# Kernel optimization log

Hardware: AMD Instinct MI355X
Metric: run time of the kernel (lower is better)

The kernel has to match this reference:

```python
import jax, jax.numpy as jnp
import numpy as np

N_NODES = 100000


def _gcn_norm(edge_index, edge_weight, n):
    # PyG gcn_norm: add self-loops (weight 1), symmetric normalization
    row, col = edge_index[0], edge_index[1]
    loop = jnp.arange(n, dtype=edge_index.dtype)
    row = jnp.concatenate([row, loop])
    col = jnp.concatenate([col, loop])
    ew = jnp.concatenate([edge_weight, jnp.ones((n,), edge_weight.dtype)])
    deg = jax.ops.segment_sum(ew, col, num_segments=n)
    dinv = jnp.where(deg > 0, jax.lax.rsqrt(deg), jnp.zeros_like(deg))
    norm = dinv[row] * ew * dinv[col]  # [E+N]
    return row, col, norm


def _gcn_layer(x, row, col, norm, W, b, n):
    h = x @ W                                   # [N, out] dense GEMM
    msg = norm[:, None] * h[row]                # gather + scale [E+N, out]
    out = jax.ops.segment_sum(msg, col, num_segments=n)  # scatter-add
    return out + b


def setup_inputs() -> dict:
    key = jax.random.key(0)
    ks = jax.random.split(key, 12)
    in_c, hid_c, out_c = 64, 128, 64
    E = 1600000
    x = jax.random.normal(ks[0], (N_NODES, in_c), jnp.float32)
    edge_index = jax.random.randint(ks[1], (2, E), 0, N_NODES, dtype=jnp.int64)
    edge_weight = jax.random.uniform(ks[2], (E,), jnp.float32)
    edge_label_index = jax.random.randint(ks[3], (2, 400000), 0, N_NODES, dtype=jnp.int64)

    def glorot(k, shape):
        lim = np.sqrt(6.0 / (shape[0] + shape[1])).astype(np.float32)
        return jax.random.uniform(k, shape, jnp.float32, -lim, lim)

    W_in = glorot(ks[4], (in_c, hid_c))
    b_in = jnp.zeros((hid_c,), jnp.float32)
    W_hid = jnp.stack([glorot(ks[5 + i], (hid_c, hid_c)) for i in range(4)])
    b_hid = jnp.zeros((4, hid_c), jnp.float32)
    W_out = glorot(ks[9], (hid_c, out_c))
    b_out = jnp.zeros((out_c,), jnp.float32)
    return {"x": x, "edge_index": edge_index, "edge_weight": edge_weight,
            "edge_label_index": edge_label_index,
            "W_in": W_in, "b_in": b_in, "W_hid": W_hid, "b_hid": b_hid,
            "W_out": W_out, "b_out": b_out}


def reference(x, edge_index, edge_weight, edge_label_index,
              W_in, b_in, W_hid, b_hid, W_out, b_out):
    n = x.shape[0]
    row, col, norm = _gcn_norm(edge_index, edge_weight, n)  # shared by all layers
    h = jax.nn.relu(_gcn_layer(x, row, col, norm, W_in, b_in, n))
    for i in range(W_hid.shape[0]):  # 4 hidden GCN layers
        h = jax.nn.relu(_gcn_layer(h, row, col, norm, W_hid[i], b_hid[i], n))
    enc = _gcn_layer(h, row, col, norm, W_out, b_out, n)  # [N, out_c]
    # dot-product link decoder
    logits = jnp.sum(enc[edge_label_index[0]] * enc[edge_label_index[1]], axis=1)
    return jax.nn.sigmoid(logits)
```

## Files before the change

### kernel.cpp

```cpp
#include <hip/hip_runtime.h>
#include <hip/hip_bf16.h>
#include <math.h>


using bf16x8 = __attribute__((ext_vector_type(8))) short;
using f32x4  = __attribute__((ext_vector_type(4))) float;

__device__ inline unsigned f2bf_bits(float f) {
    unsigned u = __float_as_uint(f);
    return (u + 0x7fffu + ((u >> 16) & 1u)) >> 16;
}
__device__ inline float bflo(unsigned w) { return __uint_as_float(w << 16); }
__device__ inline float bfhi(unsigned w) { return __uint_as_float(w & 0xffff0000u); }


__global__ void k_zero(int* __restrict__ hist, int n) {
    int i = blockIdx.x * 256 + threadIdx.x;
    if (i < n) hist[i] = 0;
}

__global__ void k_hist(const int* __restrict__ col, int* __restrict__ hist,
                       int* __restrict__ pos, int E) {
    int i = blockIdx.x * 256 + threadIdx.x;
    if (i < E) pos[i] = atomicAdd(&hist[col[i]], 1);
}

__global__ __launch_bounds__(256) void k_scan1(const int* __restrict__ hist,
                                               int* __restrict__ rowptr,
                                               int* __restrict__ bsum, int n) {
    __shared__ int lds[256];
    int t = threadIdx.x;
    int idx = blockIdx.x * 256 + t;
    int v = (idx < n) ? hist[idx] : 0;
    lds[t] = v; __syncthreads();
    for (int off = 1; off < 256; off <<= 1) {
        int x = (t >= off) ? lds[t - off] : 0;
        __syncthreads();
        lds[t] += x;
        __syncthreads();
    }
    if (idx < n) rowptr[idx] = lds[t] - v;
    if (t == 255) bsum[blockIdx.x] = lds[255];
}

__global__ __launch_bounds__(256) void k_scan2(const int* __restrict__ bsum,
                                               int* __restrict__ boff, int nb,
                                               int* __restrict__ rowptr, int n) {
    __shared__ int lds[256];
    int t = threadIdx.x;
    int carry = 0;
    for (int base = 0; base < nb; base += 256) {
        int v = (base + t < nb) ? bsum[base + t] : 0;
        lds[t] = v; __syncthreads();
        for (int off = 1; off < 256; off <<= 1) {
            int x = (t >= off) ? lds[t - off] : 0;
            __syncthreads();
            lds[t] += x;
            __syncthreads();
        }
        if (base + t < nb) boff[base + t] = carry + lds[t] - v;
        carry += lds[255];
        __syncthreads();
    }
    if (t == 0) rowptr[n] = carry;
}

__global__ void k_scan3(int* __restrict__ rowptr, const int* __restrict__ boff, int n) {
    int i = blockIdx.x * 256 + threadIdx.x;
    if (i < n) rowptr[i] += boff[blockIdx.x];
}

__global__ void k_place(const int* __restrict__ row, const int* __restrict__ col,
                        const float* __restrict__ ew, const int* __restrict__ rowptr,
                        const int* __restrict__ pos, int2* __restrict__ pairs, int E) {
    int e = blockIdx.x * 256 + threadIdx.x;
    if (e >= E) return;
    int c = col[e];
    int slot = rowptr[c] + pos[e];
    pairs[slot] = make_int2(row[e], __float_as_int(ew[e]));
}

__global__ void k_deg(const int2* __restrict__ pairs, const int* __restrict__ rowptr,
                      float* __restrict__ dinv, int n) {
    int t = blockIdx.x * 256 + threadIdx.x;
    int g = t >> 2, sub = t & 3;
    if (g >= n) return;
    int s = rowptr[g], e = rowptr[g + 1];
    float acc = 0.f;
    for (int i = s + sub; i < e; i += 4) acc += __int_as_float(pairs[i].y);
    acc += __shfl_xor(acc, 1, 4);
    acc += __shfl_xor(acc, 2, 4);
    if (sub == 0) dinv[g] = rsqrtf(1.f + acc);
}

__global__ void k_wtall(const float* __restrict__ W_in, const float* __restrict__ W_hid,
                        const float* __restrict__ W_out,
                        unsigned short* __restrict__ wt_in,
                        unsigned short* __restrict__ wt_hid,
                        unsigned short* __restrict__ wt_out) {
    int i = blockIdx.x * 256 + threadIdx.x;
    if (i < 8192) {
        int k = i / 128, nn = i % 128;
        wt_in[nn * 64 + k] = (unsigned short)f2bf_bits(W_in[i]);
    } else if (i < 73728) {
        int j = i - 8192;
        int l = j >> 14, r = j & 16383;
        int k = r / 128, nn = r % 128;
        wt_hid[l * 16384 + nn * 128 + k] = (unsigned short)f2bf_bits(W_hid[j]);
    } else if (i < 81920) {
        int j = i - 73728;
        int k = j / 64, nn = j % 64;
        wt_out[nn * 128 + k] = (unsigned short)f2bf_bits(W_out[j]);
    }
}

template <int K, int N, bool IN_BF16>
__global__ __launch_bounds__(256, 2) void k_gemm_mfma(
    const void* __restrict__ Xv, const unsigned short* __restrict__ Wt,
    unsigned short* __restrict__ H, int n)
{
    constexpr int NREP = N / 16;
    constexpr int KC   = K / 8;
    __shared__ char lds[128 * K * 2 + N * K * 2];
    char* Xs = lds;
    char* Ws = lds + 128 * K * 2;

    const int row0 = blockIdx.x * 128;
    const int tid  = threadIdx.x;

    for (int c = tid; c < 128 * KC; c += 256) {
        int r = c / KC, kc = c % KC;
        int gr = row0 + r;
        bf16x8 v = {0, 0, 0, 0, 0, 0, 0, 0};
        if (gr < n) {
            if constexpr (IN_BF16) {
                v = *(const bf16x8*)((const unsigned short*)Xv + (size_t)gr * K + kc * 8);
            } else {
                const float* xp = (const float*)Xv + (size_t)gr * K + kc * 8;
                float4 a = *(const float4*)xp;
                float4 b = *(const float4*)(xp + 4);
                v[0] = (short)f2bf_bits(a.x); v[1] = (short)f2bf_bits(a.y);
                v[2] = (short)f2bf_bits(a.z); v[3] = (short)f2bf_bits(a.w);
                v[4] = (short)f2bf_bits(b.x); v[5] = (short)f2bf_bits(b.y);
                v[6] = (short)f2bf_bits(b.z); v[7] = (short)f2bf_bits(b.w);
            }
        }
        *(bf16x8*)(Xs + ((r * (K * 2) + kc * 16) ^ ((r & 7) << 4))) = v;
    }
    for (int c = tid; c < N * KC; c += 256) {
        int r = c / KC, kc = c % KC;
        bf16x8 v = *(const bf16x8*)(Wt + (size_t)r * K + kc * 8);
        *(bf16x8*)(Ws + ((r * (K * 2) + kc * 16) ^ ((r & 7) << 4))) = v;
    }
    __syncthreads();

    const int wv   = tid >> 6;
    const int lane = tid & 63;
    const int lr   = lane & 15;
    const int lk   = lane >> 4;

    f32x4 acc[2][NREP];
    #pragma unroll
    for (int m = 0; m < 2; m++)
        #pragma unroll
        for (int j = 0; j < NREP; j++)
            acc[m][j] = (f32x4){0.f, 0.f, 0.f, 0.f};

    #pragma unroll
    for (int kk = 0; kk < K / 32; kk++) {
        int kc = kk * 4 + lk;
        bf16x8 af[2];
        #pragma unroll
        for (int m = 0; m < 2; m++) {
            int r = wv * 32 + m * 16 + lr;
            af[m] = *(const bf16x8*)(Xs + ((r * (K * 2) + kc * 16) ^ ((r & 7) << 4)));
        }
        #pragma unroll
        for (int j = 0; j < NREP; j++) {
            int r = j * 16 + lr;
            bf16x8 bfr = *(const bf16x8*)(Ws + ((r * (K * 2) + kc * 16) ^ ((r & 7) << 4)));
            acc[0][j] = __builtin_amdgcn_mfma_f32_16x16x32_bf16(af[0], bfr, acc[0][j], 0, 0, 0);
            acc[1][j] = __builtin_amdgcn_mfma_f32_16x16x32_bf16(af[1], bfr, acc[1][j], 0, 0, 0);
        }
    }

    #pragma unroll
    for (int m = 0; m < 2; m++) {
        #pragma unroll
        for (int j = 0; j < NREP; j++) {
            #pragma unroll
            for (int rr = 0; rr < 4; rr++) {
                int gr = row0 + wv * 32 + m * 16 + lk * 4 + rr;
                if (gr < n)
                    H[(size_t)gr * N + j * 16 + lr] = (unsigned short)f2bf_bits(acc[m][j][rr]);
            }
        }
    }
}

template <bool RELU>
__global__ __launch_bounds__(256) void k_aggregate128(
    const unsigned short* __restrict__ H, const int2* __restrict__ pairs,
    const int* __restrict__ rowptr, const float* __restrict__ dinv,
    const float* __restrict__ bias, unsigned* __restrict__ Out, int n)
{
    const int lane = threadIdx.x & 63;
    const int w    = threadIdx.x >> 6;
    int nd = blockIdx.x * 4 + w;
    if (nd >= n) return;
    int s  = rowptr[nd];
    int en = rowptr[nd + 1];
    float d  = dinv[nd];
    float d2 = d * d;

    const unsigned* Hu = (const unsigned*)H;
    unsigned sw = Hu[(size_t)nd * 64 + lane];
    float ax = d2 * bflo(sw), ay = d2 * bfhi(sw);
    int e = s;
    for (; e + 8 <= en; e += 8) {
        int2 pp[8]; float dv[8]; unsigned gv[8];
        #pragma unroll
        for (int u = 0; u < 8; u++) pp[u] = pairs[e + u];
        #pragma unroll
        for (int u = 0; u < 8; u++) dv[u] = dinv[pp[u].x];
        #pragma unroll
        for (int u = 0; u < 8; u++) gv[u] = Hu[(size_t)pp[u].x * 64 + lane];
        #pragma unroll
        for (int u = 0; u < 8; u++) {
            float nm = dv[u] * __int_as_float(pp[u].y) * d;
            ax = fmaf(nm, bflo(gv[u]), ax);
            ay = fmaf(nm, bfhi(gv[u]), ay);
        }
    }
    for (; e < en; e++) {
        int2 p = pairs[e];
        float nm = dinv[p.x] * __int_as_float(p.y) * d;
        unsigned g = Hu[(size_t)p.x * 64 + lane];
        ax = fmaf(nm, bflo(g), ax);
        ay = fmaf(nm, bfhi(g), ay);
    }
    float2 bb = reinterpret_cast<const float2*>(bias)[lane];
    ax += bb.x; ay += bb.y;
    if (RELU) { ax = fmaxf(ax, 0.f); ay = fmaxf(ay, 0.f); }
    Out[(size_t)nd * 64 + lane] = f2bf_bits(ax) | (f2bf_bits(ay) << 16);
}

__global__ __launch_bounds__(256) void k_aggregate64(
    const unsigned short* __restrict__ H, const int2* __restrict__ pairs,
    const int* __restrict__ rowptr, const float* __restrict__ dinv,
    const float* __restrict__ bias, unsigned* __restrict__ Out, int n)
{
    const int lane = threadIdx.x & 63;
    const int w    = threadIdx.x >> 6;
    const int li   = lane & 31;
    int nd = (blockIdx.x * 4 + w) * 2 + (lane >> 5);
    if (nd >= n) return;
    int s  = rowptr[nd];
    int en = rowptr[nd + 1];
    float d  = dinv[nd];
    float d2 = d * d;

    const unsigned* Hu = (const unsigned*)H;
    unsigned sw = Hu[(size_t)nd * 32 + li];
    float ax = d2 * bflo(sw), ay = d2 * bfhi(sw);
    int e = s;
    for (; e + 8 <= en; e += 8) {
        int2 pp[8]; float dv[8]; unsigned gv[8];
        #pragma unroll
        for (int u = 0; u < 8; u++) pp[u] = pairs[e + u];
        #pragma unroll
        for (int u = 0; u < 8; u++) dv[u] = dinv[pp[u].x];
        #pragma unroll
        for (int u = 0; u < 8; u++) gv[u] = Hu[(size_t)pp[u].x * 32 + li];
        #pragma unroll
        for (int u = 0; u < 8; u++) {
            float nm = dv[u] * __int_as_float(pp[u].y) * d;
            ax = fmaf(nm, bflo(gv[u]), ax);
            ay = fmaf(nm, bfhi(gv[u]), ay);
        }
    }
    for (; e < en; e++) {
        int2 p = pairs[e];
        float nm = dinv[p.x] * __int_as_float(p.y) * d;
        unsigned g = Hu[(size_t)p.x * 32 + li];
        ax = fmaf(nm, bflo(g), ax);
        ay = fmaf(nm, bfhi(g), ay);
    }
    float2 bb = reinterpret_cast<const float2*>(bias)[li];
    ax += bb.x; ay += bb.y;
    Out[(size_t)nd * 32 + li] = f2bf_bits(ax) | (f2bf_bits(ay) << 16);
}

__global__ void k_decode(const unsigned short* __restrict__ enc,
                         const int* __restrict__ eli, int M, float* __restrict__ out)
{
    int gid  = blockIdx.x * 256 + threadIdx.x;
    int pair = gid >> 3;
    int l    = gid & 7;
    if (pair >= M) return;
    int a = eli[pair];
    int b = eli[M + pair];
    const uint4* E4 = (const uint4*)enc;
    uint4 va = E4[(size_t)a * 8 + l];
    uint4 vb = E4[(size_t)b * 8 + l];
    float s = 0.f;
    s = fmaf(bflo(va.x), bflo(vb.x), s); s = fmaf(bfhi(va.x), bfhi(vb.x), s);
    s = fmaf(bflo(va.y), bflo(vb.y), s); s = fmaf(bfhi(va.y), bfhi(vb.y), s);
    s = fmaf(bflo(va.z), bflo(vb.z), s); s = fmaf(bfhi(va.z), bfhi(vb.z), s);
    s = fmaf(bflo(va.w), bflo(vb.w), s); s = fmaf(bfhi(va.w), bfhi(vb.w), s);
    s += __shfl_xor(s, 4, 8);
    s += __shfl_xor(s, 2, 8);
    s += __shfl_xor(s, 1, 8);
    if (l == 0) out[pair] = 1.f / (1.f + expf(-s));
}

extern "C" void kernel_launch(void* const* d_in, const int* in_sizes, int n_in,
                              void* d_out, int out_size, void* d_ws, size_t ws_size,
                              hipStream_t stream)
{
    const float* x     = (const float*)d_in[0];
    const int*   ei    = (const int*)d_in[1];
    const float* ew    = (const float*)d_in[2];
    const int*   eli   = (const int*)d_in[3];
    const float* W_in  = (const float*)d_in[4];
    const float* b_in  = (const float*)d_in[5];
    const float* W_hid = (const float*)d_in[6];
    const float* b_hid = (const float*)d_in[7];
    const float* W_out = (const float*)d_in[8];
    const float* b_out = (const float*)d_in[9];

    const int n = in_sizes[0] / 64;
    const int E = in_sizes[1] / 2;
    const int M = in_sizes[3] / 2;
    const int* row = ei;
    const int* col = ei + E;

    const int NB   = (n + 255) / 256;
    const int nb_E = (E + 255) / 256;
    const int gb   = (n + 127) / 128;
    const int ab   = (n + 3) / 4;

    char* basep = (char*)d_ws;
    size_t off = 0;
    auto alloc = [&](size_t bytes) {
        char* p = basep + off; off = (off + bytes + 255) & ~(size_t)255; return p; };
    float* dinv   = (float*)alloc((size_t)n * 4);
    int*   hist   = (int*)  alloc((size_t)n * 4);
    int*   rowptr = (int*)  alloc((size_t)(n + 1) * 4);
    int*   pos    = (int*)  alloc((size_t)E * 4);
    int*   bsum   = (int*)  alloc(1024 * 4);
    int*   boff   = (int*)  alloc(1024 * 4);
    int2*  pairs  = (int2*) alloc((size_t)E * 8);
    unsigned short* wt_in  = (unsigned short*)alloc((size_t)128 * 64 * 2);
    unsigned short* wt_hid = (unsigned short*)alloc((size_t)4 * 128 * 128 * 2);
    unsigned short* wt_out = (unsigned short*)alloc((size_t)64 * 128 * 2);
    unsigned short* Hbf    = (unsigned short*)alloc((size_t)n * 128 * 2);
    unsigned short* Abf    = (unsigned short*)alloc((size_t)n * 128 * 2);
    unsigned short* enc    = (unsigned short*)alloc((size_t)n * 64 * 2);

    k_zero<<<NB, 256, 0, stream>>>(hist, n);
    k_hist<<<nb_E, 256, 0, stream>>>(col, hist, pos, E);
    k_scan1<<<NB, 256, 0, stream>>>(hist, rowptr, bsum, n);
    k_scan2<<<1, 256, 0, stream>>>(bsum, boff, NB, rowptr, n);
    k_scan3<<<NB, 256, 0, stream>>>(rowptr, boff, n);
    k_place<<<nb_E, 256, 0, stream>>>(row, col, ew, rowptr, pos, pairs, E);
    k_deg<<<(n * 4 + 255) / 256, 256, 0, stream>>>(pairs, rowptr, dinv, n);

    k_wtall<<<320, 256, 0, stream>>>(W_in, W_hid, W_out, wt_in, wt_hid, wt_out);

    k_gemm_mfma<64, 128, false><<<gb, 256, 0, stream>>>(x, wt_in, Hbf, n);
    k_aggregate128<true><<<ab, 256, 0, stream>>>(Hbf, pairs, rowptr, dinv, b_in,
                                                 (unsigned*)Abf, n);

    for (int i = 0; i < 4; i++) {
        k_gemm_mfma<128, 128, true><<<gb, 256, 0, stream>>>(
            Abf, wt_hid + (size_t)i * 128 * 128, Hbf, n);
        k_aggregate128<true><<<ab, 256, 0, stream>>>(
            Hbf, pairs, rowptr, dinv, b_hid + (size_t)i * 128, (unsigned*)Abf, n);
    }

    k_gemm_mfma<128, 64, true><<<gb, 256, 0, stream>>>(Abf, wt_out, Hbf, n);
    k_aggregate64<<<(n + 7) / 8, 256, 0, stream>>>(Hbf, pairs, rowptr, dinv, b_out,
                                                   (unsigned*)enc, n);

    k_decode<<<(M * 8 + 255) / 256, 256, 0, stream>>>(enc, eli, M, (float*)d_out);
}
```

Before: 672.0 us.

## Premultiply source dinv into edge weights, reorder first layer, prefetch edge pairs

Folds the source-node dinv factor into the CSR edge weights once, so the aggregation kernels no longer do a dependent dinv gather per edge, and applies the destination dinv once at the end. The first layer is reordered to aggregate the 64-wide bf16 input before the GEMM (A·X·W instead of A·(X·W)), which halves the gather width for that layer; bias and ReLU move into a GEMM epilogue. The aggregation loops also software-prefetch the next batch of 8 edge pairs to overlap index loads with feature gathers. This adds a premultiply pass, an x-to-bf16 conversion kernel and extra register pressure, and it rounds x to bf16 before aggregation.

After: 725.9 us. +8.0%, slower.

```diff
diff --git a/kernel.cpp b/kernel.cpp
--- a/kernel.cpp
+++ b/kernel.cpp
@@ -91,6 +91,26 @@
     acc += __shfl_xor(acc, 1, 4);
     acc += __shfl_xor(acc, 2, 4);
     if (sub == 0) dinv[g] = rsqrtf(1.f + acc);
+}
+
+__global__ void k_premul(int2* __restrict__ pairs, const float* __restrict__ dinv, int E) {
+    int e = blockIdx.x * 256 + threadIdx.x;
+    if (e >= E) return;
+    int2 p = pairs[e];
+    pairs[e] = make_int2(p.x, __float_as_int(dinv[p.x] * __int_as_float(p.y)));
+}
+
+__global__ void k_xbf(const float* __restrict__ x, unsigned short* __restrict__ xb,
+                      long total4) {
+    long i = (long)blockIdx.x * 256 + threadIdx.x;
+    if (i >= total4) return;
+    float4 v = reinterpret_cast<const float4*>(x)[i];
+    ushort4 o;
+    o.x = (unsigned short)f2bf_bits(v.x);
+    o.y = (unsigned short)f2bf_bits(v.y);
+    o.z = (unsigned short)f2bf_bits(v.z);
+    o.w = (unsigned short)f2bf_bits(v.w);
+    reinterpret_cast<ushort4*>(xb)[i] = o;
 }
 
 __global__ void k_wtall(const float* __restrict__ W_in, const float* __restrict__ W_hid,
@@ -114,10 +134,10 @@
     }
 }
 
-template <int K, int N, bool IN_BF16>
+template <int K, int N, bool IN_BF16, bool EPI>
 __global__ __launch_bounds__(256, 2) void k_gemm_mfma(
     const void* __restrict__ Xv, const unsigned short* __restrict__ Wt,
-    unsigned short* __restrict__ H, int n)
+    const float* __restrict__ bias, unsigned short* __restrict__ H, int n)
 {
     constexpr int NREP = N / 16;
     constexpr int KC   = K / 8;
@@ -188,11 +208,15 @@
     for (int m = 0; m < 2; m++) {
         #pragma unroll
         for (int j = 0; j < NREP; j++) {
+            float bcol = EPI ? bias[j * 16 + lr] : 0.f;
             #pragma unroll
             for (int rr = 0; rr < 4; rr++) {
                 int gr = row0 + wv * 32 + m * 16 + lk * 4 + rr;
-                if (gr < n)
-                    H[(size_t)gr * N + j * 16 + lr] = (unsigned short)f2bf_bits(acc[m][j][rr]);
+                if (gr < n) {
+                    float v = acc[m][j][rr];
+                    if constexpr (EPI) v = fmaxf(v + bcol, 0.f);
+                    H[(size_t)gr * N + j * 16 + lr] = (unsigned short)f2bf_bits(v);
+                }
             }
         }
     }
@@ -210,41 +234,55 @@
     if (nd >= n) return;
     int s  = rowptr[nd];
     int en = rowptr[nd + 1];
-    float d  = dinv[nd];
-    float d2 = d * d;
+    float d = dinv[nd];
 
     const unsigned* Hu = (const unsigned*)H;
     unsigned sw = Hu[(size_t)nd * 64 + lane];
-    float ax = d2 * bflo(sw), ay = d2 * bfhi(sw);
+    float ax = d * bflo(sw), ay = d * bfhi(sw);
+
     int e = s;
-    for (; e + 8 <= en; e += 8) {
-        int2 pp[8]; float dv[8]; unsigned gv[8];
-        #pragma unroll
-        for (int u = 0; u < 8; u++) pp[u] = pairs[e + u];
-        #pragma unroll
-        for (int u = 0; u < 8; u++) dv[u] = dinv[pp[u].x];
-        #pragma unroll
-        for (int u = 0; u < 8; u++) gv[u] = Hu[(size_t)pp[u].x * 64 + lane];
+    int2 ppA[8];
+    bool haveA = (e + 8 <= en);
+    if (haveA) {
+        #pragma unroll
+        for (int u = 0; u < 8; u++) ppA[u] = pairs[e + u];
+    }
+    while (haveA) {
+        int enext = e + 8;
+        int2 ppB[8];
+        bool haveB = (enext + 8 <= en);
+        if (haveB) {
+            #pragma unroll
+            for (int u = 0; u < 8; u++) ppB[u] = pairs[enext + u];
+        }
+        unsigned gv[8];
+        #pragma unroll
+        for (int u = 0; u < 8; u++) gv[u] = Hu[(size_t)ppA[u].x * 64 + lane];
         #pragma unroll
         for (int u = 0; u < 8; u++) {
-            float nm = dv[u] * __int_as_float(pp[u].y) * d;
+            float nm = __int_as_float(ppA[u].y);
             ax = fmaf(nm, bflo(gv[u]), ax);
             ay = fmaf(nm, bfhi(gv[u]), ay);
         }
+        #pragma unroll
+        for (int u = 0; u < 8; u++) ppA[u] = ppB[u];
+        e = enext; haveA = haveB;
     }
     for (; e < en; e++) {
         int2 p = pairs[e];
-        float nm = dinv[p.x] * __int_as_float(p.y) * d;
         unsigned g = Hu[(size_t)p.x * 64 + lane];
+        float nm = __int_as_float(p.y);
         ax = fmaf(nm, bflo(g), ax);
         ay = fmaf(nm, bfhi(g), ay);
     }
     float2 bb = reinterpret_cast<const float2*>(bias)[lane];
-    ax += bb.x; ay += bb.y;
+    ax = d * ax + bb.x;
+    ay = d * ay + bb.y;
     if (RELU) { ax = fmaxf(ax, 0.f); ay = fmaxf(ay, 0.f); }
     Out[(size_t)nd * 64 + lane] = f2bf_bits(ax) | (f2bf_bits(ay) << 16);
 }
 
+template <bool BIAS>
 __global__ __launch_bounds__(256) void k_aggregate64(
     const unsigned short* __restrict__ H, const int2* __restrict__ pairs,
     const int* __restrict__ rowptr, const float* __restrict__ dinv,
@@ -257,37 +295,55 @@
     if (nd >= n) return;
     int s  = rowptr[nd];
     int en = rowptr[nd + 1];
-    float d  = dinv[nd];
-    float d2 = d * d;
+    float d = dinv[nd];
 
     const unsigned* Hu = (const unsigned*)H;
     unsigned sw = Hu[(size_t)nd * 32 + li];
-    float ax = d2 * bflo(sw), ay = d2 * bfhi(sw);
+    float ax = d * bflo(sw), ay = d * bfhi(sw);
+
     int e = s;
-    for (; e + 8 <= en; e += 8) {
-        int2 pp[8]; float dv[8]; unsigned gv[8];
-        #pragma unroll
-        for (int u = 0; u < 8; u++) pp[u] = pairs[e + u];
-        #pragma unroll
-        for (int u = 0; u < 8; u++) dv[u] = dinv[pp[u].x];
-        #pragma unroll
-        for (int u = 0; u < 8; u++) gv[u] = Hu[(size_t)pp[u].x * 32 + li];
+    int2 ppA[8];
+    bool haveA = (e + 8 <= en);
+    if (haveA) {
+        #pragma unroll
+        for (int u = 0; u < 8; u++) ppA[u] = pairs[e + u];
+    }
+    while (haveA) {
+        int enext = e + 8;
+        int2 ppB[8];
+        bool haveB = (enext + 8 <= en);
+        if (haveB) {
+            #pragma unroll
+            for (int u = 0; u < 8; u++) ppB[u] = pairs[enext + u];
+        }
+        unsigned gv[8];
+        #pragma unroll
+        for (int u = 0; u < 8; u++) gv[u] = Hu[(size_t)ppA[u].x * 32 + li];
         #pragma unroll
         for (int u = 0; u < 8; u++) {
-            float nm = dv[u] * __int_as_float(pp[u].y) * d;
+            float nm = __int_as_float(ppA[u].y);
             ax = fmaf(nm, bflo(gv[u]), ax);
             ay = fmaf(nm, bfhi(gv[u]), ay);
         }
+        #pragma unroll
+        for (int u = 0; u < 8; u++) ppA[u] = ppB[u];
+        e = enext; haveA = haveB;
     }
     for (; e < en; e++) {
         int2 p = pairs[e];
-        float nm = dinv[p.x] * __int_as_float(p.y) * d;
         unsigned g = Hu[(size_t)p.x * 32 + li];
+        float nm = __int_as_float(p.y);
         ax = fmaf(nm, bflo(g), ax);
         ay = fmaf(nm, bfhi(g), ay);
     }
-    float2 bb = reinterpret_cast<const float2*>(bias)[li];
-    ax += bb.x; ay += bb.y;
+    if constexpr (BIAS) {
+        float2 bb = reinterpret_cast<const float2*>(bias)[li];
+        ax = d * ax + bb.x;
+        ay = d * ay + bb.y;
+    } else {
+        ax = d * ax;
+        ay = d * ay;
+    }
     Out[(size_t)nd * 32 + li] = f2bf_bits(ax) | (f2bf_bits(ay) << 16);
 }
 
@@ -354,6 +410,7 @@
     unsigned short* wt_in  = (unsigned short*)alloc((size_t)128 * 64 * 2);
     unsigned short* wt_hid = (unsigned short*)alloc((size_t)4 * 128 * 128 * 2);
     unsigned short* wt_out = (unsigned short*)alloc((size_t)64 * 128 * 2);
+    unsigned short* xb     = (unsigned short*)alloc((size_t)n * 64 * 2);
     unsigned short* Hbf    = (unsigned short*)alloc((size_t)n * 128 * 2);
     unsigned short* Abf    = (unsigned short*)alloc((size_t)n * 128 * 2);
     unsigned short* enc    = (unsigned short*)alloc((size_t)n * 64 * 2);
@@ -365,23 +422,27 @@
     k_scan3<<<NB, 256, 0, stream>>>(rowptr, boff, n);
     k_place<<<nb_E, 256, 0, stream>>>(row, col, ew, rowptr, pos, pairs, E);
     k_deg<<<(n * 4 + 255) / 256, 256, 0, stream>>>(pairs, rowptr, dinv, n);
+    k_premul<<<nb_E, 256, 0, stream>>>(pairs, dinv, E);
 
     k_wtall<<<320, 256, 0, stream>>>(W_in, W_hid, W_out, wt_in, wt_hid, wt_out);
-
-    k_gemm_mfma<64, 128, false><<<gb, 256, 0, stream>>>(x, wt_in, Hbf, n);
-    k_aggregate128<true><<<ab, 256, 0, stream>>>(Hbf, pairs, rowptr, dinv, b_in,
-                                                 (unsigned*)Abf, n);
+    k_xbf<<<(int)(((long)n * 16 + 255) / 256), 256, 0, stream>>>(x, xb, (long)n * 16);
+
+    k_aggregate64<false><<<(n + 7) / 8, 256, 0, stream>>>(
+        xb, pairs, rowptr, dinv, nullptr, (unsigned*)Hbf, n);
+    k_gemm_mfma<64, 128, true, true><<<gb, 256, 0, stream>>>(
+        Hbf, wt_in, b_in, Abf, n);
 
     for (int i = 0; i < 4; i++) {
-        k_gemm_mfma<128, 128, true><<<gb, 256, 0, stream>>>(
-            Abf, wt_hid + (size_t)i * 128 * 128, Hbf, n);
+        k_gemm_mfma<128, 128, true, false><<<gb, 256, 0, stream>>>(
+            Abf, wt_hid + (size_t)i * 128 * 128, nullptr, Hbf, n);
         k_aggregate128<true><<<ab, 256, 0, stream>>>(
             Hbf, pairs, rowptr, dinv, b_hid + (size_t)i * 128, (unsigned*)Abf, n);
     }
 
-    k_gemm_mfma<128, 64, true><<<gb, 256, 0, stream>>>(Abf, wt_out, Hbf, n);
-    k_aggregate64<<<(n + 7) / 8, 256, 0, stream>>>(Hbf, pairs, rowptr, dinv, b_out,
-                                                   (unsigned*)enc, n);
+    k_gemm_mfma<128, 64, true, false><<<gb, 256, 0, stream>>>(
+        Abf, wt_out, nullptr, Hbf, n);
+    k_aggregate64<true><<<(n + 7) / 8, 256, 0, stream>>>(
+        Hbf, pairs, rowptr, dinv, b_out, (unsigned*)enc, n);
 
     k_decode<<<(M * 8 + 255) / 256, 256, 0, stream>>>(enc, eli, M, (float*)d_out);
 }
```
